# Kernel tuning notes

Measured on AMD Instinct MI355X. Metric: run time of the kernel, lower is better.

The kernel has to match this reference:

```python
import jax, jax.numpy as jnp
import numpy as np

B, S = 32, 4096
Q_DIM, KV_DIM, A_DIM = 512, 512, 128


def setup_inputs() -> dict:
    key = jax.random.key(0)
    k1, k2, k3, k4, k5, k6 = jax.random.split(key, 6)
    query = jax.random.normal(k1, (B, Q_DIM), dtype=jnp.float32)
    kv = jax.random.normal(k2, (B, S, KV_DIM), dtype=jnp.float32)
    mask = jax.random.randint(k3, (B, S), 0, 2).astype(bool)
    # learned params (torch Linear(in, out, bias=False) stores W as [out, in]; we apply x @ W.T)
    Wq = jax.random.normal(k4, (A_DIM, Q_DIM), dtype=jnp.float32) / np.sqrt(Q_DIM)
    Wk = jax.random.normal(k5, (A_DIM, KV_DIM), dtype=jnp.float32) / np.sqrt(KV_DIM)
    Ws = jax.random.normal(k6, (1, A_DIM), dtype=jnp.float32) / np.sqrt(A_DIM)
    return {"query": query, "kv": kv, "mask": mask, "Wq": Wq, "Wk": Wk, "Ws": Ws}


def reference(query, kv, mask, Wq, Wk, Ws):
    # q: [B, 1, A], k: [B, S, A]
    q = jnp.einsum('bq,aq->ba', query, Wq)[:, None, :]
    k = jnp.einsum('bsk,ak->bsa', kv, Wk)
    # additive (Bahdanau) scores: [B, S]
    scores = jnp.einsum('bsa,a->bs', jnp.tanh(q + k), Ws[0])
    scores = jnp.where(mask, scores, -jnp.inf)
    weights = jax.nn.softmax(scores, axis=-1)
    context = jnp.einsum('bs,bsk->bk', weights, kv)
    return context, weights
```

## Files before the change

### kernel.cpp

```cpp
#include <hip/hip_runtime.h>


typedef __attribute__((ext_vector_type(8))) short short8;
typedef __attribute__((ext_vector_type(4))) float f32x4;

#define S_LEN 4096
#define BATCH 32
#define KVD 512
#define AD 128
#define SCHN 32
#define CHUNKS_PER_B (S_LEN / SCHN)
#define NCHUNK (BATCH * CHUNKS_PER_B)

#define FLAG_OFF   0
#define Q_OFF      1024
#define WK_OFF     17408
#define SCORES_OFF 148480
#define MD_OFF     672768
#define CTXP_OFF   705536

__device__ __forceinline__ unsigned short f2bf(float f) {
  unsigned int u = __float_as_uint(f);
  u = (u + 0x7FFFu + ((u >> 16) & 1u)) >> 16;
  return (unsigned short)u;
}
__device__ __forceinline__ float bf2f(unsigned short h) {
  return __uint_as_float(((unsigned int)h) << 16);
}
__device__ __forceinline__ float tanh_fast(float x) {
  return 1.0f - 2.0f / (1.0f + __expf(2.0f * x));
}

__global__ __launch_bounds__(256) void prep_kernel(
    const float* __restrict__ query, const float* __restrict__ Wq,
    const float* __restrict__ Wk, const void* __restrict__ maskp,
    float* __restrict__ qws, unsigned short* __restrict__ wkb,
    int* __restrict__ flagp) {
  int blk = blockIdx.x, t = threadIdx.x;
  if (blk < 32) {
    __shared__ float qrow[KVD];
    qrow[t] = query[blk * KVD + t];
    qrow[t + 256] = query[blk * KVD + t + 256];
    __syncthreads();
    int a = t >> 1, half = t & 1;
    const float4* wq4 = (const float4*)(Wq + (size_t)a * KVD + half * 256);
    const float4* qr4 = (const float4*)(qrow + half * 256);
    float s = 0.f;
#pragma unroll 8
    for (int i = 0; i < 64; ++i) {
      float4 wv = wq4[i], qv = qr4[i];
      s += wv.x * qv.x + wv.y * qv.y + wv.z * qv.z + wv.w * qv.w;
    }
    s += __shfl_xor(s, 1);
    if (half == 0) qws[blk * AD + a] = s;
  } else if (blk < 40) {
    int j = blk - 32;
    const float4* src = (const float4*)Wk;
#pragma unroll 4
    for (int i = 0; i < 8; ++i) {
      int idx4 = j * 2048 + i * 256 + t;
      float4 v = src[idx4];
      ushort4 o;
      o.x = f2bf(v.x); o.y = f2bf(v.y); o.z = f2bf(v.z); o.w = f2bf(v.w);
      ((ushort4*)wkb)[idx4] = o;
    }
  } else {
    __shared__ int okv;
    if (t == 0) okv = 1;
    __syncthreads();
    if (t < 128) {
      int wv = ((const int*)maskp)[t];
      if (!(wv == 0 || wv == 1)) okv = 0;
    }
    __syncthreads();
    if (t == 0) flagp[0] = okv;
  }
}

__global__ __launch_bounds__(256) void main_kernel(
    const float* __restrict__ kv, const void* __restrict__ maskp,
    const float* __restrict__ Ws, const float* __restrict__ qws,
    const unsigned short* __restrict__ wkb, const int* __restrict__ flagp,
    float* __restrict__ scores, float* __restrict__ md,
    float* __restrict__ ctxp) {
  int blk = blockIdx.x, t = threadIdx.x;
  int b = blk >> 7, chunk = blk & 127;
  int s0 = chunk * SCHN;

  __shared__ unsigned short kvb[SCHN][520];
  __shared__ float qs[AD], wss[AD];
  __shared__ float scp[4][SCHN];
  __shared__ float esc[SCHN];

  if (t < AD) { qs[t] = qws[b * AD + t]; wss[t] = Ws[t]; }

  const float4* kvv = (const float4*)(kv + (size_t)b * S_LEN * KVD + (size_t)s0 * KVD);
#pragma unroll 4
  for (int i = 0; i < 16; ++i) {
    int idx4 = t + 256 * i;
    float4 v = kvv[idx4];
    int c4 = idx4 << 2;
    int r = c4 >> 9, c = c4 & 511;
    uint2 pk;
    pk.x = (unsigned)f2bf(v.x) | ((unsigned)f2bf(v.y) << 16);
    pk.y = (unsigned)f2bf(v.z) | ((unsigned)f2bf(v.w) << 16);
    *(uint2*)&kvb[r][c] = pk;
  }
  __syncthreads();

  int lane = t & 63, wave = t >> 6;
  int lr = lane & 15, lg = lane >> 4;
  int a0 = wave * 32;
  f32x4 acc[2][2];
#pragma unroll
  for (int mi = 0; mi < 2; ++mi)
#pragma unroll
    for (int ni = 0; ni < 2; ++ni) acc[mi][ni] = (f32x4)0.f;

#pragma unroll 4
  for (int kk = 0; kk < KVD / 32; ++kk) {
    int kb = kk * 32 + lg * 8;
    short8 af0 = *(const short8*)&kvb[lr][kb];
    short8 af1 = *(const short8*)&kvb[16 + lr][kb];
    short8 bf0 = *(const short8*)(wkb + (size_t)(a0 + lr) * KVD + kb);
    short8 bf1 = *(const short8*)(wkb + (size_t)(a0 + 16 + lr) * KVD + kb);
    acc[0][0] = __builtin_amdgcn_mfma_f32_16x16x32_bf16(af0, bf0, acc[0][0], 0, 0, 0);
    acc[1][0] = __builtin_amdgcn_mfma_f32_16x16x32_bf16(af1, bf0, acc[1][0], 0, 0, 0);
    acc[0][1] = __builtin_amdgcn_mfma_f32_16x16x32_bf16(af0, bf1, acc[0][1], 0, 0, 0);
    acc[1][1] = __builtin_amdgcn_mfma_f32_16x16x32_bf16(af1, bf1, acc[1][1], 0, 0, 0);
  }

#pragma unroll
  for (int mi = 0; mi < 2; ++mi) {
#pragma unroll
    for (int reg = 0; reg < 4; ++reg) {
      float v = 0.f;
#pragma unroll
      for (int ni = 0; ni < 2; ++ni) {
        int a = a0 + ni * 16 + lr;
        float x = qs[a] + acc[mi][ni][reg];
        v += tanh_fast(x) * wss[a];
      }
      v += __shfl_xor(v, 1);
      v += __shfl_xor(v, 2);
      v += __shfl_xor(v, 4);
      v += __shfl_xor(v, 8);
      if (lr == 0) scp[wave][mi * 16 + lg * 4 + reg] = v;
    }
  }
  __syncthreads();

  if (t < SCHN) {
    float sm = scp[0][t] + scp[1][t] + scp[2][t] + scp[3][t];
    int gs = s0 + t;
    int flag = flagp[0];
    int mk = flag ? ((const int*)maskp)[b * S_LEN + gs]
                  : (int)((const unsigned char*)maskp)[b * S_LEN + gs];
    float score = mk ? sm : -INFINITY;
    scores[b * S_LEN + gs] = score;
    float m = score;
    m = fmaxf(m, __shfl_xor(m, 16));
    m = fmaxf(m, __shfl_xor(m, 8));
    m = fmaxf(m, __shfl_xor(m, 4));
    m = fmaxf(m, __shfl_xor(m, 2));
    m = fmaxf(m, __shfl_xor(m, 1));
    float e = (score == -INFINITY) ? 0.f : __expf(score - m);
    float d = e;
    d += __shfl_xor(d, 16);
    d += __shfl_xor(d, 8);
    d += __shfl_xor(d, 4);
    d += __shfl_xor(d, 2);
    d += __shfl_xor(d, 1);
    esc[t] = e;
    if (t == 0) { md[blk * 2] = m; md[blk * 2 + 1] = d; }
  }
  __syncthreads();

  {
    float c0 = 0.f, c1 = 0.f;
#pragma unroll 4
    for (int s = 0; s < SCHN; ++s) {
      float e = esc[s];
      unsigned int u = *(const unsigned int*)&kvb[s][2 * t];
      c0 += e * bf2f((unsigned short)u);
      c1 += e * bf2f((unsigned short)(u >> 16));
    }
    ctxp[(size_t)blk * KVD + 2 * t] = c0;
    ctxp[(size_t)blk * KVD + 2 * t + 1] = c1;
  }
}

__global__ __launch_bounds__(512) void combine_kernel(
    const float* __restrict__ md, const float* __restrict__ ctxp,
    const float* __restrict__ scores, float* __restrict__ out) {
  int b = blockIdx.x, t = threadIdx.x;
  __shared__ float mv[CHUNKS_PER_B], dv[CHUNKS_PER_B], scl[CHUNKS_PER_B];
  __shared__ float Msh, Dsh;
  if (t < CHUNKS_PER_B) {
    mv[t] = md[(b * CHUNKS_PER_B + t) * 2];
    dv[t] = md[(b * CHUNKS_PER_B + t) * 2 + 1];
  }
  __syncthreads();
  if (t < 64) {
    float m = fmaxf(mv[t], mv[t + 64]);
    m = fmaxf(m, __shfl_xor(m, 32));
    m = fmaxf(m, __shfl_xor(m, 16));
    m = fmaxf(m, __shfl_xor(m, 8));
    m = fmaxf(m, __shfl_xor(m, 4));
    m = fmaxf(m, __shfl_xor(m, 2));
    m = fmaxf(m, __shfl_xor(m, 1));
    if (t == 0) Msh = m;
  }
  __syncthreads();
  float M = Msh;
  if (t < CHUNKS_PER_B) scl[t] = (dv[t] > 0.f) ? __expf(mv[t] - M) : 0.f;
  __syncthreads();
  if (t < 64) {
    float d = scl[t] * dv[t] + scl[t + 64] * dv[t + 64];
    d += __shfl_xor(d, 32);
    d += __shfl_xor(d, 16);
    d += __shfl_xor(d, 8);
    d += __shfl_xor(d, 4);
    d += __shfl_xor(d, 2);
    d += __shfl_xor(d, 1);
    if (t == 0) Dsh = d;
  }
  __syncthreads();
  float invD = 1.f / Dsh;
  for (int c = t; c < KVD; c += 512) {
    float sum = 0.f;
#pragma unroll 4
    for (int j = 0; j < CHUNKS_PER_B; ++j)
      sum += scl[j] * ctxp[(size_t)(b * CHUNKS_PER_B + j) * KVD + c];
    out[b * KVD + c] = sum * invD;
  }
  for (int s = t; s < S_LEN; s += 512) {
    float sc = scores[b * S_LEN + s];
    out[BATCH * KVD + b * S_LEN + s] = __expf(sc - M) * invD;
  }
}

extern "C" void kernel_launch(void* const* d_in, const int* in_sizes, int n_in,
                              void* d_out, int out_size, void* d_ws, size_t ws_size,
                              hipStream_t stream) {
  const float* query = (const float*)d_in[0];
  const float* kv    = (const float*)d_in[1];
  const void*  maskp = d_in[2];
  const float* Wq    = (const float*)d_in[3];
  const float* Wk    = (const float*)d_in[4];
  const float* Ws    = (const float*)d_in[5];
  float* out = (float*)d_out;
  char* w = (char*)d_ws;
  int* flagp = (int*)(w + FLAG_OFF);
  float* qws = (float*)(w + Q_OFF);
  unsigned short* wkb = (unsigned short*)(w + WK_OFF);
  float* scores = (float*)(w + SCORES_OFF);
  float* md = (float*)(w + MD_OFF);
  float* ctxp = (float*)(w + CTXP_OFF);

  prep_kernel<<<41, 256, 0, stream>>>(query, Wq, Wk, maskp, qws, wkb, flagp);
  main_kernel<<<NCHUNK, 256, 0, stream>>>(kv, maskp, Ws, qws, wkb, flagp,
                                          scores, md, ctxp);
  combine_kernel<<<BATCH, 512, 0, stream>>>(md, ctxp, scores, out);
}
```

Measured before the change: 127.2 us.

## Give each wave its own 32-row chunk, drop LDS staging of kv

Each wave now handles a whole 32-row sequence chunk across all 128 attention columns, so the block count falls by four. The kv tile is no longer staged as bf16 in LDS: MFMA A-fragments are loaded from global and converted in registers, and the context sum rereads kv in fp32 from global, counting on cache hits. The goal is to cut the LDS footprint, most block-level barriers and the cross-wave score reduction. The cost is a second read of kv, more Wk fragment loads per wave and heavier register pressure from 16 accumulators under a 3-block occupancy hint.

After: 144.7 us. 13.8% more time.

```diff
diff --git a/kernel.cpp b/kernel.cpp
--- a/kernel.cpp
+++ b/kernel.cpp
@@ -24,11 +24,16 @@
   u = (u + 0x7FFFu + ((u >> 16) & 1u)) >> 16;
   return (unsigned short)u;
 }
-__device__ __forceinline__ float bf2f(unsigned short h) {
-  return __uint_as_float(((unsigned int)h) << 16);
-}
 __device__ __forceinline__ float tanh_fast(float x) {
   return 1.0f - 2.0f / (1.0f + __expf(2.0f * x));
+}
+__device__ __forceinline__ short8 pack8(float4 lo, float4 hi) {
+  short8 r;
+  r[0] = (short)f2bf(lo.x); r[1] = (short)f2bf(lo.y);
+  r[2] = (short)f2bf(lo.z); r[3] = (short)f2bf(lo.w);
+  r[4] = (short)f2bf(hi.x); r[5] = (short)f2bf(hi.y);
+  r[6] = (short)f2bf(hi.z); r[7] = (short)f2bf(hi.w);
+  return r;
 }
 
 __global__ __launch_bounds__(256) void prep_kernel(
@@ -77,117 +82,126 @@
   }
 }
 
-__global__ __launch_bounds__(256) void main_kernel(
+__global__ __launch_bounds__(256, 3) void main_kernel(
     const float* __restrict__ kv, const void* __restrict__ maskp,
     const float* __restrict__ Ws, const float* __restrict__ qws,
     const unsigned short* __restrict__ wkb, const int* __restrict__ flagp,
     float* __restrict__ scores, float* __restrict__ md,
     float* __restrict__ ctxp) {
-  int blk = blockIdx.x, t = threadIdx.x;
-  int b = blk >> 7, chunk = blk & 127;
+  int t = threadIdx.x;
+  int lane = t & 63, wave = t >> 6;
+  int g = blockIdx.x * 4 + wave;
+  int b = g >> 7, chunk = g & 127;
   int s0 = chunk * SCHN;
-
-  __shared__ unsigned short kvb[SCHN][520];
-  __shared__ float qs[AD], wss[AD];
-  __shared__ float scp[4][SCHN];
-  __shared__ float esc[SCHN];
-
-  if (t < AD) { qs[t] = qws[b * AD + t]; wss[t] = Ws[t]; }
-
-  const float4* kvv = (const float4*)(kv + (size_t)b * S_LEN * KVD + (size_t)s0 * KVD);
-#pragma unroll 4
-  for (int i = 0; i < 16; ++i) {
-    int idx4 = t + 256 * i;
-    float4 v = kvv[idx4];
-    int c4 = idx4 << 2;
-    int r = c4 >> 9, c = c4 & 511;
-    uint2 pk;
-    pk.x = (unsigned)f2bf(v.x) | ((unsigned)f2bf(v.y) << 16);
-    pk.y = (unsigned)f2bf(v.z) | ((unsigned)f2bf(v.w) << 16);
-    *(uint2*)&kvb[r][c] = pk;
-  }
-  __syncthreads();
-
-  int lane = t & 63, wave = t >> 6;
   int lr = lane & 15, lg = lane >> 4;
-  int a0 = wave * 32;
-  f32x4 acc[2][2];
+
+  __shared__ float esc[4][SCHN];
+  __shared__ float ssc[4][SCHN];
+
+  const float* arow0 = kv + ((size_t)b * S_LEN + s0 + lr) * KVD + lg * 8;
+  const float* arow1 = arow0 + (size_t)16 * KVD;
+  const unsigned short* brow = wkb + (size_t)lr * KVD + lg * 8;
+
+  f32x4 acc[2][8];
 #pragma unroll
   for (int mi = 0; mi < 2; ++mi)
 #pragma unroll
-    for (int ni = 0; ni < 2; ++ni) acc[mi][ni] = (f32x4)0.f;
-
-#pragma unroll 4
+    for (int n = 0; n < 8; ++n) acc[mi][n] = (f32x4)0.f;
+
   for (int kk = 0; kk < KVD / 32; ++kk) {
-    int kb = kk * 32 + lg * 8;
-    short8 af0 = *(const short8*)&kvb[lr][kb];
-    short8 af1 = *(const short8*)&kvb[16 + lr][kb];
-    short8 bf0 = *(const short8*)(wkb + (size_t)(a0 + lr) * KVD + kb);
-    short8 bf1 = *(const short8*)(wkb + (size_t)(a0 + 16 + lr) * KVD + kb);
-    acc[0][0] = __builtin_amdgcn_mfma_f32_16x16x32_bf16(af0, bf0, acc[0][0], 0, 0, 0);
-    acc[1][0] = __builtin_amdgcn_mfma_f32_16x16x32_bf16(af1, bf0, acc[1][0], 0, 0, 0);
-    acc[0][1] = __builtin_amdgcn_mfma_f32_16x16x32_bf16(af0, bf1, acc[0][1], 0, 0, 0);
-    acc[1][1] = __builtin_amdgcn_mfma_f32_16x16x32_bf16(af1, bf1, acc[1][1], 0, 0, 0);
-  }
-
+    int ko = kk * 32;
+    float4 a0lo = *(const float4*)(arow0 + ko);
+    float4 a0hi = *(const float4*)(arow0 + ko + 4);
+    float4 a1lo = *(const float4*)(arow1 + ko);
+    float4 a1hi = *(const float4*)(arow1 + ko + 4);
+    short8 bfr[8];
+#pragma unroll
+    for (int n = 0; n < 8; ++n)
+      bfr[n] = *(const short8*)(brow + (size_t)n * 16 * KVD + ko);
+    short8 af0 = pack8(a0lo, a0hi);
+    short8 af1 = pack8(a1lo, a1hi);
+#pragma unroll
+    for (int n = 0; n < 8; ++n) {
+      acc[0][n] = __builtin_amdgcn_mfma_f32_16x16x32_bf16(af0, bfr[n], acc[0][n], 0, 0, 0);
+      acc[1][n] = __builtin_amdgcn_mfma_f32_16x16x32_bf16(af1, bfr[n], acc[1][n], 0, 0, 0);
+    }
+  }
+
+  float qv[8], wv[8];
+#pragma unroll
+  for (int n = 0; n < 8; ++n) {
+    qv[n] = qws[b * AD + n * 16 + lr];
+    wv[n] = Ws[n * 16 + lr];
+  }
+  int flag = flagp[0];
+  float sc[2][4];
 #pragma unroll
   for (int mi = 0; mi < 2; ++mi) {
 #pragma unroll
     for (int reg = 0; reg < 4; ++reg) {
       float v = 0.f;
 #pragma unroll
-      for (int ni = 0; ni < 2; ++ni) {
-        int a = a0 + ni * 16 + lr;
-        float x = qs[a] + acc[mi][ni][reg];
-        v += tanh_fast(x) * wss[a];
-      }
+      for (int n = 0; n < 8; ++n)
+        v += tanh_fast(qv[n] + acc[mi][n][reg]) * wv[n];
       v += __shfl_xor(v, 1);
       v += __shfl_xor(v, 2);
       v += __shfl_xor(v, 4);
       v += __shfl_xor(v, 8);
-      if (lr == 0) scp[wave][mi * 16 + lg * 4 + reg] = v;
-    }
-  }
-  __syncthreads();
-
-  if (t < SCHN) {
-    float sm = scp[0][t] + scp[1][t] + scp[2][t] + scp[3][t];
-    int gs = s0 + t;
-    int flag = flagp[0];
-    int mk = flag ? ((const int*)maskp)[b * S_LEN + gs]
-                  : (int)((const unsigned char*)maskp)[b * S_LEN + gs];
-    float score = mk ? sm : -INFINITY;
-    scores[b * S_LEN + gs] = score;
-    float m = score;
-    m = fmaxf(m, __shfl_xor(m, 16));
-    m = fmaxf(m, __shfl_xor(m, 8));
-    m = fmaxf(m, __shfl_xor(m, 4));
-    m = fmaxf(m, __shfl_xor(m, 2));
-    m = fmaxf(m, __shfl_xor(m, 1));
-    float e = (score == -INFINITY) ? 0.f : __expf(score - m);
-    float d = e;
-    d += __shfl_xor(d, 16);
-    d += __shfl_xor(d, 8);
-    d += __shfl_xor(d, 4);
-    d += __shfl_xor(d, 2);
-    d += __shfl_xor(d, 1);
-    esc[t] = e;
-    if (t == 0) { md[blk * 2] = m; md[blk * 2 + 1] = d; }
-  }
-  __syncthreads();
-
-  {
-    float c0 = 0.f, c1 = 0.f;
+      int gs = b * S_LEN + s0 + 16 * mi + 4 * lg + reg;
+      int mk = flag ? ((const int*)maskp)[gs]
+                    : (int)((const unsigned char*)maskp)[gs];
+      sc[mi][reg] = mk ? v : -INFINITY;
+    }
+  }
+
+  float m = -INFINITY;
+#pragma unroll
+  for (int mi = 0; mi < 2; ++mi)
+#pragma unroll
+    for (int reg = 0; reg < 4; ++reg) m = fmaxf(m, sc[mi][reg]);
+  m = fmaxf(m, __shfl_xor(m, 16));
+  m = fmaxf(m, __shfl_xor(m, 32));
+  float e[2][4];
+  float d = 0.f;
+#pragma unroll
+  for (int mi = 0; mi < 2; ++mi)
+#pragma unroll
+    for (int reg = 0; reg < 4; ++reg) {
+      e[mi][reg] = (sc[mi][reg] == -INFINITY) ? 0.f : __expf(sc[mi][reg] - m);
+      d += e[mi][reg];
+    }
+  d += __shfl_xor(d, 16);
+  d += __shfl_xor(d, 32);
+
+  if (lr == 0) {
+#pragma unroll
+    for (int mi = 0; mi < 2; ++mi)
+#pragma unroll
+      for (int reg = 0; reg < 4; ++reg) {
+        int srow = 16 * mi + 4 * lg + reg;
+        esc[wave][srow] = e[mi][reg];
+        ssc[wave][srow] = sc[mi][reg];
+      }
+  }
+  if (lane == 0) { md[g * 2] = m; md[g * 2 + 1] = d; }
+  __syncthreads();
+
+  if (lane < SCHN) scores[b * S_LEN + s0 + lane] = ssc[wave][lane];
+
+  float4 c0 = make_float4(0.f, 0.f, 0.f, 0.f);
+  float4 c1 = make_float4(0.f, 0.f, 0.f, 0.f);
+  const float* kvc = kv + ((size_t)b * S_LEN + s0) * KVD + lane * 8;
 #pragma unroll 4
-    for (int s = 0; s < SCHN; ++s) {
-      float e = esc[s];
-      unsigned int u = *(const unsigned int*)&kvb[s][2 * t];
-      c0 += e * bf2f((unsigned short)u);
-      c1 += e * bf2f((unsigned short)(u >> 16));
-    }
-    ctxp[(size_t)blk * KVD + 2 * t] = c0;
-    ctxp[(size_t)blk * KVD + 2 * t + 1] = c1;
-  }
+  for (int s = 0; s < SCHN; ++s) {
+    float ev = esc[wave][s];
+    float4 v0 = *(const float4*)(kvc + (size_t)s * KVD);
+    float4 v1 = *(const float4*)(kvc + (size_t)s * KVD + 4);
+    c0.x += ev * v0.x; c0.y += ev * v0.y; c0.z += ev * v0.z; c0.w += ev * v0.w;
+    c1.x += ev * v1.x; c1.y += ev * v1.y; c1.z += ev * v1.z; c1.w += ev * v1.w;
+  }
+  float* cp = ctxp + (size_t)g * KVD + lane * 8;
+  *(float4*)cp = c0;
+  *(float4*)(cp + 4) = c1;
 }
 
 __global__ __launch_bounds__(512) void combine_kernel(
@@ -259,7 +273,7 @@
   float* ctxp = (float*)(w + CTXP_OFF);
 
   prep_kernel<<<41, 256, 0, stream>>>(query, Wq, Wk, maskp, qws, wkb, flagp);
-  main_kernel<<<NCHUNK, 256, 0, stream>>>(kv, maskp, Ws, qws, wkb, flagp,
-                                          scores, md, ctxp);
+  main_kernel<<<NCHUNK / 4, 256, 0, stream>>>(kv, maskp, Ws, qws, wkb, flagp,
+                                              scores, md, ctxp);
   combine_kernel<<<BATCH, 512, 0, stream>>>(md, ctxp, scores, out);
 }
```
